# Kernel optimization log

Measured on AMD Instinct MI355X. Metric: run time of the kernel, lower is better.

Reference implementation:

```python
import jax, jax.numpy as jnp
import numpy as np

N_NODES = 100000
N_EDGES = 1600000


def gcn_conv(x, W, b, src, dst, n_nodes):
    # PyG GCNConv: h = X W; out_i = sum_j norm_ij * h_j + b, with
    # norm_ij = deg_i^{-1/2} deg_j^{-1/2} over A + I (self-loops already appended).
    h = x @ W                                   # [N, F_out]
    deg = jax.ops.segment_sum(jnp.ones(src.shape[0], x.dtype), dst,
                              num_segments=n_nodes)          # [N]
    dinv = jax.lax.rsqrt(jnp.maximum(deg, 1.0))              # deg >= 1 (self-loops)
    norm = dinv[src] * dinv[dst]                             # [E]
    msg = h[src] * norm[:, None]                             # gather + scale
    out = jax.ops.segment_sum(msg, dst, num_segments=n_nodes)
    return out + b


def setup_inputs() -> dict:
    key = jax.random.key(0)
    k1, k2, k3, k4 = jax.random.split(key, 4)
    x = jax.random.normal(k1, (N_NODES, 500), dtype=jnp.float32)
    edge_index = jax.random.randint(k2, (2, N_EDGES), 0, N_NODES, dtype=jnp.int64)
    W1 = jax.random.normal(k3, (500, 64), dtype=jnp.float32) * (1.0 / np.sqrt(500))
    b1 = jnp.zeros((64,), dtype=jnp.float32)
    W2 = jax.random.normal(k4, (64, 40), dtype=jnp.float32) * (1.0 / np.sqrt(64))
    b2 = jnp.zeros((40,), dtype=jnp.float32)
    return {"x": x, "edge_index": edge_index, "W1": W1, "b1": b1, "W2": W2, "b2": b2}


def reference(x, edge_index, W1, b1, W2, b2):
    n = x.shape[0]
    loops = jnp.arange(n, dtype=edge_index.dtype)
    src = jnp.concatenate([edge_index[0], loops])
    dst = jnp.concatenate([edge_index[1], loops])
    h = jax.nn.relu(gcn_conv(x, W1, b1, src, dst, n))
    # dropout is identity in eval mode (training=False)
    h = gcn_conv(h, W2, b2, src, dst, n)
    return jax.nn.log_softmax(h, axis=1)
```

## Files before the change

kernel.cpp:

```cpp
#include <hip/hip_runtime.h>
#include <hip/hip_bf16.h>
#include <math.h>

#define NNODES 100000
#define F_IN   500
#define F_MID  64
#define F_OUT  40
#define KPAD   512
#define H2S    48

#define BSH    7
#define NBUCK  782
#define EPB    8192
#define K4CACHE 3072

typedef __attribute__((ext_vector_type(8))) short short8;
typedef __attribute__((ext_vector_type(4))) float f32x4;

__device__ __forceinline__ unsigned short f2bf(float f) {
    union { float f; unsigned u; } c; c.f = f;
    unsigned r = c.u + 0x7FFF + ((c.u >> 16) & 1);
    return (unsigned short)(r >> 16);
}
__device__ __forceinline__ float bf2f(unsigned short u) {
    union { unsigned v; float f; } c; c.v = ((unsigned)u) << 16; return c.f;
}


__global__ __launch_bounds__(256) void bucket_count(const int* __restrict__ dst,
                                                    int* __restrict__ bcnt, int E) {
    __shared__ int h[NBUCK];
    int tid = threadIdx.x;
    for (int b = tid; b < NBUCK; b += 256) h[b] = 0;
    __syncthreads();
    int base = blockIdx.x * EPB;
#pragma unroll
    for (int j = 0; j < EPB / 256; j++) {
        int e = base + j * 256 + tid;
        if (e < E) atomicAdd(&h[dst[e] >> BSH], 1);
    }
    __syncthreads();
    for (int b = tid; b < NBUCK; b += 256) {
        int c = h[b];
        if (c) atomicAdd(&bcnt[b], c);
    }
}

__global__ __launch_bounds__(1024) void bucket_scan(const int* __restrict__ bcnt,
                                                    int* __restrict__ bstart,
                                                    int* __restrict__ bcur, int E) {
    __shared__ int wsum[16];
    int t = threadIdx.x, lane = t & 63, w = t >> 6;
    int v = (t < NBUCK) ? bcnt[t] : 0;
    int s = v;
#pragma unroll
    for (int off = 1; off < 64; off <<= 1) {
        int u = __shfl_up(s, off, 64);
        if (lane >= off) s += u;
    }
    if (lane == 63) wsum[w] = s;
    __syncthreads();
    if (w == 0) {
        int ws = (lane < 16) ? wsum[lane] : 0;
#pragma unroll
        for (int off = 1; off < 16; off <<= 1) {
            int u = __shfl_up(ws, off, 64);
            if (lane >= off) ws += u;
        }
        if (lane < 16) wsum[lane] = ws;
    }
    __syncthreads();
    int excl = s - v + ((w > 0) ? wsum[w - 1] : 0);
    if (t < NBUCK) { bstart[t] = excl; bcur[t] = excl; }
    if (t == 0) bstart[NBUCK] = E;
}

__global__ __launch_bounds__(256) void bucket_scatter(const int* __restrict__ src,
                                                      const int* __restrict__ dst,
                                                      int* __restrict__ bcur,
                                                      int* __restrict__ stage, int E) {
    __shared__ int h[NBUCK];
    __shared__ int lcur[NBUCK];
    int tid = threadIdx.x;
    for (int b = tid; b < NBUCK; b += 256) h[b] = 0;
    __syncthreads();
    int base = blockIdx.x * EPB;
#pragma unroll
    for (int j = 0; j < EPB / 256; j++) {
        int e = base + j * 256 + tid;
        if (e < E) atomicAdd(&h[dst[e] >> BSH], 1);
    }
    __syncthreads();
    int rot = (blockIdx.x * 97) % NBUCK;
    for (int i = tid; i < NBUCK; i += 256) {
        int b = i + rot; if (b >= NBUCK) b -= NBUCK;
        int c = h[b];
        lcur[b] = c ? atomicAdd(&bcur[b], c) : 0;
    }
    __syncthreads();
#pragma unroll
    for (int j = 0; j < EPB / 256; j++) {
        int e = base + j * 256 + tid;
        if (e < E) {
            int d = dst[e];
            int pos = atomicAdd(&lcur[d >> BSH], 1);
            stage[pos] = ((d & 127) << 17) | src[e];
        }
    }
}

__global__ __launch_bounds__(256) void bucket_fill(const int* __restrict__ stage,
                                                   const int* __restrict__ bstart,
                                                   int* __restrict__ row_start,
                                                   float* __restrict__ dinv,
                                                   int* __restrict__ csr_src, int E) {
    __shared__ int cnt[128];
    __shared__ int wtot[2];
    __shared__ int cache[K4CACHE];
    int tid = threadIdx.x;
    int b = blockIdx.x;
    int s0 = bstart[b], s1 = bstart[b + 1];
    int nE = s1 - s0;
    if (tid < 128) cnt[tid] = 0;
    __syncthreads();
    bool cached = (nE <= K4CACHE);
    for (int i = tid; i < nE; i += 256) {
        int v = stage[s0 + i];
        if (cached) cache[i] = v;
        atomicAdd(&cnt[v >> 17], 1);
    }
    __syncthreads();
    int n = (b << BSH) + tid;
    bool valid = (tid < 128) && (n < NNODES);
    int c = (tid < 128) ? cnt[tid] : 0;
    int add = valid ? (c + 1) : 0;
    int s = add;
    int lane = tid & 63;
#pragma unroll
    for (int off = 1; off < 64; off <<= 1) {
        int u = __shfl_up(s, off, 64);
        if (lane >= off) s += u;
    }
    if (tid < 128 && lane == 63) wtot[tid >> 6] = s;
    __syncthreads();
    int excl = s - add + ((tid >= 64 && tid < 128) ? wtot[0] : 0);
    int basep = s0 + (b << BSH) + excl;
    if (valid) {
        row_start[n] = basep;
        dinv[n] = rsqrtf((float)(c + 1));
        csr_src[basep] = n;
        cnt[tid] = basep + 1;
    }
    if (b == NBUCK - 1 && tid == 0) row_start[NNODES] = E + NNODES;
    __syncthreads();
    for (int i = tid; i < nE; i += 256) {
        int v = cached ? cache[i] : stage[s0 + i];
        int pos = atomicAdd(&cnt[v >> 17], 1);
        csr_src[pos] = v & 0x1FFFF;
    }
}

__global__ void w1t_prep(const float* __restrict__ W1, unsigned short* __restrict__ W1T) {
    int idx = blockIdx.x * blockDim.x + threadIdx.x;
    if (idx >= F_MID * KPAD) return;
    int n = idx >> 9;
    int k = idx & (KPAD - 1);
    float v = (k < F_IN) ? W1[k * F_MID + n] : 0.f;
    W1T[idx] = f2bf(v);
}

__global__ void w2t_prep(const float* __restrict__ W2, unsigned short* __restrict__ W2T) {
    int idx = blockIdx.x * blockDim.x + threadIdx.x;
    if (idx >= H2S * F_MID) return;
    int c = idx >> 6;
    int k = idx & 63;
    float v = (c < F_OUT) ? W2[k * F_OUT + c] : 0.f;
    W2T[idx] = f2bf(v);
}

__global__ __launch_bounds__(256, 4) void gemm1_kernel(const float* __restrict__ X,
                                                       const unsigned short* __restrict__ W1T,
                                                       const float* __restrict__ dinv,
                                                       unsigned short* __restrict__ h1b) {
    int tid = threadIdx.x;
    int wave = tid >> 6;
    int lane = tid & 63;
    int m = lane & 15, quad = lane >> 4;
    int n0 = blockIdx.x * 64 + wave * 16;

    int arow = n0 + m; if (arow >= NNODES) arow = NNODES - 1;
    const float* xrow = X + (size_t)arow * F_IN;

    f32x4 acc[4];
#pragma unroll
    for (int c = 0; c < 4; c++) { f32x4 z = {0.f, 0.f, 0.f, 0.f}; acc[c] = z; }

    const int NK = KPAD / 32;
#pragma unroll 4
    for (int ks = 0; ks < NK; ks++) {
        int kg = ks * 32 + quad * 8;
        float4 a0, a1;
        if (kg < F_IN)     a0 = *(const float4*)(xrow + kg);
        else               a0 = make_float4(0.f, 0.f, 0.f, 0.f);
        if (kg + 4 < F_IN) a1 = *(const float4*)(xrow + kg + 4);
        else               a1 = make_float4(0.f, 0.f, 0.f, 0.f);

        unsigned pk[4];
        pk[0] = (unsigned)f2bf(a0.x) | ((unsigned)f2bf(a0.y) << 16);
        pk[1] = (unsigned)f2bf(a0.z) | ((unsigned)f2bf(a0.w) << 16);
        pk[2] = (unsigned)f2bf(a1.x) | ((unsigned)f2bf(a1.y) << 16);
        pk[3] = (unsigned)f2bf(a1.z) | ((unsigned)f2bf(a1.w) << 16);
        short8 a;
        *(unsigned*)&((short*)&a)[0] = pk[0];
        *(unsigned*)&((short*)&a)[2] = pk[1];
        *(unsigned*)&((short*)&a)[4] = pk[2];
        *(unsigned*)&((short*)&a)[6] = pk[3];

#pragma unroll
        for (int c = 0; c < 4; c++) {
            short8 b = *(const short8*)&W1T[(size_t)(c * 16 + m) * KPAD + ks * 32 + quad * 8];
            acc[c] = __builtin_amdgcn_mfma_f32_16x16x32_bf16(a, b, acc[c], 0, 0, 0);
        }
    }

#pragma unroll
    for (int reg = 0; reg < 4; reg++) {
        int gr = n0 + quad * 4 + reg;
        if (gr < NNODES) {
            float sc = dinv[gr];
#pragma unroll
            for (int c = 0; c < 4; c++)
                h1b[(size_t)gr * F_MID + c * 16 + m] = f2bf(acc[c][reg] * sc);
        }
    }
}

__global__ __launch_bounds__(256) void agg1_kernel(const unsigned short* __restrict__ h1b,
                                                   const int* __restrict__ csr_src,
                                                   const int* __restrict__ row_start,
                                                   const float* __restrict__ dinv,
                                                   const float* __restrict__ b1,
                                                   unsigned short* __restrict__ out1b) {
    int tid = threadIdx.x;
    int node = blockIdx.x * 4 + (tid >> 6);
    int lane = tid & 63;

    int s0 = row_start[node], s1 = row_start[node + 1];
    float acc = 0.f;

    int idx[8];
    int e = s0;
#pragma unroll
    for (int j = 0; j < 8; j++) {
        int p = e + j; if (p > s1 - 1) p = s1 - 1;
        idx[j] = csr_src[p];
    }
    while (e < s1) {
        int cnt = s1 - e;
        int cidx[8];
#pragma unroll
        for (int j = 0; j < 8; j++) cidx[j] = idx[j];
        int en = e + 8;
        if (en < s1) {
#pragma unroll
            for (int j = 0; j < 8; j++) {
                int p = en + j; if (p > s1 - 1) p = s1 - 1;
                idx[j] = csr_src[p];
            }
        }
#pragma unroll
        for (int j = 0; j < 8; j++) {
            float v = bf2f(h1b[(size_t)cidx[j] * F_MID + lane]);
            if (j < cnt) acc += v;
        }
        e = en;
    }

    float dn = dinv[node];
    float v = fmaxf(acc * dn + b1[lane], 0.f);
    out1b[(size_t)node * F_MID + lane] = f2bf(v);
}

__global__ __launch_bounds__(256) void gemm2_kernel(const unsigned short* __restrict__ out1b,
                                                    const unsigned short* __restrict__ W2T,
                                                    const float* __restrict__ dinv,
                                                    unsigned short* __restrict__ h2b) {
    int tid = threadIdx.x;
    int wave = tid >> 6;
    int lane = tid & 63;
    int n0 = blockIdx.x * 64 + wave * 16;
    int m = lane & 15, quad = lane >> 4;

    int arow = n0 + m; if (arow >= NNODES) arow = NNODES - 1;

    f32x4 acc[3];
#pragma unroll
    for (int c = 0; c < 3; c++) { f32x4 z = {0.f, 0.f, 0.f, 0.f}; acc[c] = z; }

#pragma unroll
    for (int t = 0; t < 2; t++) {
        short8 a = *(const short8*)&out1b[(size_t)arow * F_MID + t * 32 + quad * 8];
#pragma unroll
        for (int c = 0; c < 3; c++) {
            short8 b = *(const short8*)&W2T[(size_t)(c * 16 + m) * F_MID + t * 32 + quad * 8];
            acc[c] = __builtin_amdgcn_mfma_f32_16x16x32_bf16(a, b, acc[c], 0, 0, 0);
        }
    }

#pragma unroll
    for (int reg = 0; reg < 4; reg++) {
        int gr = n0 + quad * 4 + reg;
        if (gr < NNODES) {
            float dn = dinv[gr];
#pragma unroll
            for (int c = 0; c < 3; c++)
                h2b[(size_t)gr * H2S + c * 16 + m] = f2bf(acc[c][reg] * dn);
        }
    }
}

__global__ __launch_bounds__(256) void agg2_softmax_kernel(const unsigned short* __restrict__ h2b,
                                                           const int* __restrict__ csr_src,
                                                           const int* __restrict__ row_start,
                                                           const float* __restrict__ dinv,
                                                           const float* __restrict__ b2,
                                                           float* __restrict__ out) {
    int tid = threadIdx.x;
    int node = blockIdx.x * 4 + (tid >> 6);
    int lane = tid & 63;
    int cl = (lane < H2S) ? lane : 0;

    int s0 = row_start[node], s1 = row_start[node + 1];
    float acc = 0.f;

    int idx[8];
    int e = s0;
#pragma unroll
    for (int j = 0; j < 8; j++) {
        int p = e + j; if (p > s1 - 1) p = s1 - 1;
        idx[j] = csr_src[p];
    }
    while (e < s1) {
        int cnt = s1 - e;
        int cidx[8];
#pragma unroll
        for (int j = 0; j < 8; j++) cidx[j] = idx[j];
        int en = e + 8;
        if (en < s1) {
#pragma unroll
            for (int j = 0; j < 8; j++) {
                int p = en + j; if (p > s1 - 1) p = s1 - 1;
                idx[j] = csr_src[p];
            }
        }
#pragma unroll
        for (int j = 0; j < 8; j++) {
            float v = bf2f(h2b[(size_t)cidx[j] * H2S + cl]);
            if (j < cnt) acc += v;
        }
        e = en;
    }

    float dn = dinv[node];
    bool act = (lane < F_OUT);
    float z = act ? (acc * dn + b2[cl]) : -3.4e38f;
    float m = z;
#pragma unroll
    for (int off = 1; off < 64; off <<= 1) m = fmaxf(m, __shfl_xor(m, off, 64));
    float p = act ? __expf(z - m) : 0.f;
#pragma unroll
    for (int off = 1; off < 64; off <<= 1) p += __shfl_xor(p, off, 64);
    float lse = m + logf(p);
    if (act) out[(size_t)node * F_OUT + lane] = z - lse;
}

extern "C" void kernel_launch(void* const* d_in, const int* in_sizes, int n_in,
                              void* d_out, int out_size, void* d_ws, size_t ws_size,
                              hipStream_t stream) {
    const float* X   = (const float*)d_in[0];
    const int*   ei  = (const int*)d_in[1];
    const float* W1  = (const float*)d_in[2];
    const float* b1  = (const float*)d_in[3];
    const float* W2  = (const float*)d_in[4];
    const float* b2  = (const float*)d_in[5];
    float* out = (float*)d_out;

    const int N = NNODES;
    const int E = in_sizes[1] / 2;
    const int TOTAL = E + N;
    const int* srcv = ei;
    const int* dstv = ei + E;

    char* p = (char*)d_ws;
    auto carve = [&](size_t bytes) {
        void* r = (void*)p;
        p += (bytes + 255) & ~(size_t)255;
        return r;
    };
    int*   bcnt      = (int*)carve((size_t)NBUCK * 4);
    int*   bstart    = (int*)carve((size_t)(NBUCK + 1) * 4);
    int*   bcur      = (int*)carve((size_t)NBUCK * 4);
    int*   stage     = (int*)carve((size_t)E * 4);
    int*   row_start = (int*)carve((size_t)(N + 1) * 4);
    int*   csr_src   = (int*)carve((size_t)TOTAL * 4);
    float* dinv      = (float*)carve((size_t)N * 4);
    unsigned short* W1T  = (unsigned short*)carve((size_t)F_MID * KPAD * 2);
    unsigned short* W2T  = (unsigned short*)carve((size_t)H2S * F_MID * 2);
    unsigned short* h1b  = (unsigned short*)carve((size_t)N * F_MID * 2);
    unsigned short* out1b= (unsigned short*)carve((size_t)N * F_MID * 2);
    unsigned short* h2b  = (unsigned short*)carve((size_t)N * H2S * 2);
    (void)ws_size; (void)n_in; (void)out_size;

    const int GB = (E + EPB - 1) / EPB;

    hipMemsetAsync(bcnt, 0, (size_t)NBUCK * 4, stream);
    bucket_count<<<GB, 256, 0, stream>>>(dstv, bcnt, E);
    bucket_scan<<<1, 1024, 0, stream>>>(bcnt, bstart, bcur, E);
    bucket_scatter<<<GB, 256, 0, stream>>>(srcv, dstv, bcur, stage, E);
    bucket_fill<<<NBUCK, 256, 0, stream>>>(stage, bstart, row_start, dinv, csr_src, E);

    w1t_prep<<<(F_MID * KPAD + 255) / 256, 256, 0, stream>>>(W1, W1T);
    w2t_prep<<<(H2S * F_MID + 255) / 256, 256, 0, stream>>>(W2, W2T);

    gemm1_kernel<<<(N + 63) / 64, 256, 0, stream>>>(X, W1T, dinv, h1b);
    agg1_kernel<<<N / 4, 256, 0, stream>>>(h1b, csr_src, row_start, dinv, b1, out1b);
    gemm2_kernel<<<(N + 63) / 64, 256, 0, stream>>>(out1b, W2T, dinv, h2b);
    agg2_softmax_kernel<<<N / 4, 256, 0, stream>>>(h2b, csr_src, row_start, dinv, b2, out);
}
```

Before: 537.0 us.

## Stage X tile in swizzled LDS as bf16 for coalesced GEMM1 loads

```diff
diff --git a/kernel.cpp b/kernel.cpp
--- a/kernel.cpp
+++ b/kernel.cpp
@@ -178,44 +178,54 @@
     W2T[idx] = f2bf(v);
 }
 
-__global__ __launch_bounds__(256, 4) void gemm1_kernel(const float* __restrict__ X,
+__global__ __launch_bounds__(256, 2) void gemm1_kernel(const float* __restrict__ X,
                                                        const unsigned short* __restrict__ W1T,
                                                        const float* __restrict__ dinv,
                                                        unsigned short* __restrict__ h1b) {
+    __shared__ __align__(16) unsigned short A_lds[64][KPAD];
+
     int tid = threadIdx.x;
     int wave = tid >> 6;
     int lane = tid & 63;
     int m = lane & 15, quad = lane >> 4;
-    int n0 = blockIdx.x * 64 + wave * 16;
-
-    int arow = n0 + m; if (arow >= NNODES) arow = NNODES - 1;
-    const float* xrow = X + (size_t)arow * F_IN;
+    int n0 = blockIdx.x * 64;
+
+#pragma unroll 4
+    for (int r = 0; r < 16; r++) {
+        int row = wave * 16 + r;
+        int grow = n0 + row; if (grow >= NNODES) grow = NNODES - 1;
+        const float* xp = X + (size_t)grow * F_IN;
+        int sw = (row & 7) << 4;
+        char* lrow = (char*)&A_lds[row][0];
+
+        float4 v0 = *(const float4*)(xp + lane * 4);
+        unsigned p0 = (unsigned)f2bf(v0.x) | ((unsigned)f2bf(v0.y) << 16);
+        unsigned p1 = (unsigned)f2bf(v0.z) | ((unsigned)f2bf(v0.w) << 16);
+        *(uint2*)(lrow + ((lane * 8) ^ sw)) = make_uint2(p0, p1);
+
+        if (lane < 61) {
+            float4 v1 = *(const float4*)(xp + 256 + lane * 4);
+            unsigned q0 = (unsigned)f2bf(v1.x) | ((unsigned)f2bf(v1.y) << 16);
+            unsigned q1 = (unsigned)f2bf(v1.z) | ((unsigned)f2bf(v1.w) << 16);
+            *(uint2*)(lrow + ((512 + lane * 8) ^ sw)) = make_uint2(q0, q1);
+        }
+        if (lane < 6) {
+            *(unsigned*)(lrow + ((1000 + lane * 4) ^ sw)) = 0u;
+        }
+    }
+    __syncthreads();
 
     f32x4 acc[4];
 #pragma unroll
     for (int c = 0; c < 4; c++) { f32x4 z = {0.f, 0.f, 0.f, 0.f}; acc[c] = z; }
 
-    const int NK = KPAD / 32;
+    int arow = wave * 16 + m;
+    const char* lra = (const char*)&A_lds[arow][0];
+    int swr = (m & 7) << 4;
+
 #pragma unroll 4
-    for (int ks = 0; ks < NK; ks++) {
-        int kg = ks * 32 + quad * 8;
-        float4 a0, a1;
-        if (kg < F_IN)     a0 = *(const float4*)(xrow + kg);
-        else               a0 = make_float4(0.f, 0.f, 0.f, 0.f);
-        if (kg + 4 < F_IN) a1 = *(const float4*)(xrow + kg + 4);
-        else               a1 = make_float4(0.f, 0.f, 0.f, 0.f);
-
-        unsigned pk[4];
-        pk[0] = (unsigned)f2bf(a0.x) | ((unsigned)f2bf(a0.y) << 16);
-        pk[1] = (unsigned)f2bf(a0.z) | ((unsigned)f2bf(a0.w) << 16);
-        pk[2] = (unsigned)f2bf(a1.x) | ((unsigned)f2bf(a1.y) << 16);
-        pk[3] = (unsigned)f2bf(a1.z) | ((unsigned)f2bf(a1.w) << 16);
-        short8 a;
-        *(unsigned*)&((short*)&a)[0] = pk[0];
-        *(unsigned*)&((short*)&a)[2] = pk[1];
-        *(unsigned*)&((short*)&a)[4] = pk[2];
-        *(unsigned*)&((short*)&a)[6] = pk[3];
-
+    for (int ks = 0; ks < KPAD / 32; ks++) {
+        short8 a = *(const short8*)(lra + ((ks * 64 + quad * 16) ^ swr));
 #pragma unroll
         for (int c = 0; c < 4; c++) {
             short8 b = *(const short8*)&W1T[(size_t)(c * 16 + m) * KPAD + ks * 32 + quad * 8];
@@ -223,9 +233,10 @@
         }
     }
 
+    int n0w = n0 + wave * 16;
 #pragma unroll
     for (int reg = 0; reg < 4; reg++) {
-        int gr = n0 + quad * 4 + reg;
+        int gr = n0w + quad * 4 + reg;
         if (gr < NNODES) {
             float sc = dinv[gr];
 #pragma unroll
```

New measurement: 562.4 us. 1.05x slower.
